# Performance work log

Measured on AMD Instinct MI355X. Metric: run time of the kernel, lower is better.

The kernel has to match this reference:

```python
import jax, jax.numpy as jnp
import numpy as np

B, S, D, H = 4, 2048, 768, 12
DH = D // H  # 64


def setup_inputs() -> dict:
    key = jax.random.key(0)
    ks = jax.random.split(key, 7)
    return {
        "sequences": jax.random.normal(ks[0], (B, S, D), dtype=jnp.float32),
        "wq": jax.random.normal(ks[1], (H, DH, DH), dtype=jnp.float32) / np.sqrt(DH),
        "bq": jax.random.normal(ks[2], (H, DH), dtype=jnp.float32) * 0.02,
        "wk": jax.random.normal(ks[3], (H, DH, DH), dtype=jnp.float32) / np.sqrt(DH),
        "bk": jax.random.normal(ks[4], (H, DH), dtype=jnp.float32) * 0.02,
        "wv": jax.random.normal(ks[5], (H, DH, DH), dtype=jnp.float32) / np.sqrt(DH),
        "bv": jax.random.normal(ks[6], (H, DH), dtype=jnp.float32) * 0.02,
    }


def reference(sequences, wq, bq, wk, bk, wv, bv):
    # split channels into heads: [B, S, H, DH]
    xh = sequences.reshape(B, S, H, DH)
    # per-head linear projections (weight applied as x @ W^T + b, matching nn.Linear)
    q = jnp.einsum("bshd,hed->bshe", xh, wq) + bq  # [B,S,H,DH]
    k = jnp.einsum("bshd,hed->bshe", xh, wk) + bk
    v = jnp.einsum("bshd,hed->bshe", xh, wv) + bv
    scale = 1.0 / np.sqrt(DH).astype(np.float32)
    scores = jnp.einsum("bqhd,bkhd->bhqk", q, k) * scale  # [B,H,S,S]
    attn = jax.nn.softmax(scores, axis=-1)
    out = jnp.einsum("bhqk,bkhd->bqhd", attn, v)  # [B,S,H,DH]
    return out.reshape(B, S, D)
```

## Files before the change

### kernel.cpp

```cpp
#include <hip/hip_runtime.h>

#define NB 4
#define NS 2048
#define ND 768
#define NH 12
#define NDH 64
#define XPITCH 72
#define SSCALE 0.18033688011112043f

typedef __bf16 bf16x8 __attribute__((ext_vector_type(8)));
typedef float  f32x4  __attribute__((ext_vector_type(4)));
typedef unsigned int u32;

#define MFMA16(a, b, c) __builtin_amdgcn_mfma_f32_16x16x32_bf16(a, b, c, 0, 0, 0)

__device__ __forceinline__ u32 packbf(float a, float b) {
    u32 ua = __builtin_bit_cast(u32, a) + 0x8000u;
    u32 ub = __builtin_bit_cast(u32, b) + 0x8000u;
    return __builtin_amdgcn_perm(ub, ua, 0x07060302u);
}

__device__ __forceinline__ bf16x8 cvt8(float4 a, float4 b) {
    union { u32 u[4]; bf16x8 v; } r;
    r.u[0] = packbf(a.x, a.y); r.u[1] = packbf(a.z, a.w);
    r.u[2] = packbf(b.x, b.y); r.u[3] = packbf(b.z, b.w);
    return r.v;
}

__device__ __forceinline__ __bf16 f2bf(float f) {
    u32 u = __builtin_bit_cast(u32, f) + 0x8000u;
    unsigned short s = (unsigned short)(u >> 16);
    return __builtin_bit_cast(__bf16, s);
}

__device__ __forceinline__ void gl16(const __bf16* g, __bf16* l) {
    __builtin_amdgcn_global_load_lds(
        (const __attribute__((address_space(1))) unsigned int*)g,
        (__attribute__((address_space(3))) unsigned int*)l,
        16, 0, 0);
}


__global__ __launch_bounds__(256, 3) void proj_kernel(
    const float* __restrict__ x,
    const float* __restrict__ wq, const float* __restrict__ bq,
    const float* __restrict__ wk, const float* __restrict__ bk,
    const float* __restrict__ wv, const float* __restrict__ bv,
    __bf16* __restrict__ qws, __bf16* __restrict__ kws, __bf16* __restrict__ vtws)
{
    const int stp = blockIdx.x, h = blockIdx.y, b = blockIdx.z;
    const int st0 = stp * 2, st1 = stp * 2 + 1;
    const int tid = threadIdx.x;

    __shared__ __align__(16) __bf16 Xs[2][64 * XPITCH];
    __shared__ __align__(16) __bf16 Tv[2][64 * XPITCH];

    const int r = tid >> 2, f = tid & 3;
    const int lane = tid & 63, w = tid >> 6, col = lane & 15, quad = lane >> 4;

    const size_t wrow = (size_t)(h * NDH + w * 16 + col) * NDH;
    const float* wq0 = wq + wrow + quad * 8;
    const float* wk0 = wk + wrow + quad * 8;
    const float* wv0 = wv + wrow + quad * 8;
    const bf16x8 wqa0 = cvt8(*(const float4*)(wq0),      *(const float4*)(wq0 + 4));
    const bf16x8 wqa1 = cvt8(*(const float4*)(wq0 + 32), *(const float4*)(wq0 + 36));
    const bf16x8 wka0 = cvt8(*(const float4*)(wk0),      *(const float4*)(wk0 + 4));
    const bf16x8 wka1 = cvt8(*(const float4*)(wk0 + 32), *(const float4*)(wk0 + 36));
    const bf16x8 wva0 = cvt8(*(const float4*)(wv0),      *(const float4*)(wv0 + 4));
    const bf16x8 wva1 = cvt8(*(const float4*)(wv0 + 32), *(const float4*)(wv0 + 36));

    float bqs[4], bks[4], bvs[4];
#pragma unroll
    for (int rr = 0; rr < 4; ++rr) {
        const int e = h * NDH + w * 16 + quad * 4 + rr;
        bqs[rr] = bq[e] * SSCALE;
        bks[rr] = bk[e];
        bvs[rr] = bv[e];
    }

    const size_t bh = (size_t)(b * NH + h);

    const int e0 = w * 16 + quad * 4;
    const int jj = e0 >> 5;
    const int qa = (e0 >> 3) & 3;
    const int hf = (e0 >> 2) & 1;
    const int Lf = qa * 16 + col;

    const float* xrow0 = x + (size_t)(b * NS + st0 * 64 + r) * ND + h * NDH + f * 16;
    const float* xrow1 = xrow0 + (size_t)64 * ND;
    {
        const float4 v0 = *(const float4*)(xrow0);
        const float4 v1 = *(const float4*)(xrow0 + 4);
        const float4 v2 = *(const float4*)(xrow0 + 8);
        const float4 v3 = *(const float4*)(xrow0 + 12);
        *(bf16x8*)&Xs[0][r * XPITCH + f * 16]     = cvt8(v0, v1);
        *(bf16x8*)&Xs[0][r * XPITCH + f * 16 + 8] = cvt8(v2, v3);
    }
    const float4 xn0 = *(const float4*)(xrow1);
    const float4 xn1 = *(const float4*)(xrow1 + 4);
    const float4 xn2 = *(const float4*)(xrow1 + 8);
    const float4 xn3 = *(const float4*)(xrow1 + 12);
    __syncthreads();

    auto do_tile = [&](int st, const __bf16* XsP, __bf16* TvP) {
        const int kt = st >> 1;
#pragma unroll
        for (int nt = 0; nt < 4; ++nt) {
            const bf16x8 xb0 = *(const bf16x8*)&XsP[(nt * 16 + col) * XPITCH + quad * 8];
            const bf16x8 xb1 = *(const bf16x8*)&XsP[(nt * 16 + col) * XPITCH + 32 + quad * 8];
            f32x4 aq = {0.f, 0.f, 0.f, 0.f};
            f32x4 ak = {0.f, 0.f, 0.f, 0.f};
            f32x4 av = {0.f, 0.f, 0.f, 0.f};
            aq = MFMA16(wqa0, xb0, aq); aq = MFMA16(wqa1, xb1, aq);
            ak = MFMA16(wka0, xb0, ak); ak = MFMA16(wka1, xb1, ak);
            av = MFMA16(wva0, xb0, av); av = MFMA16(wva1, xb1, av);

            union { u32 u[2]; uint2 v; } pq, pk;
            pq.u[0] = packbf(fmaf(aq[0], SSCALE, bqs[0]), fmaf(aq[1], SSCALE, bqs[1]));
            pq.u[1] = packbf(fmaf(aq[2], SSCALE, bqs[2]), fmaf(aq[3], SSCALE, bqs[3]));
            pk.u[0] = packbf(ak[0] + bks[0], ak[1] + bks[1]);
            pk.u[1] = packbf(ak[2] + bks[2], ak[3] + bks[3]);

            const int wa = (st & 1) * 2 + (nt >> 1);
            const int mt = nt & 1;
            const size_t kidx = ((((((size_t)bh * 16 + kt) * 4 + wa) * 2 + mt) * 2 + jj) * 64 + Lf) * 8 + hf * 4;
            const size_t qidx = (((((size_t)bh * 32 + st) * 4 + nt) * 2 + jj) * 64 + Lf) * 8 + hf * 4;
            *(uint2*)(kws + kidx) = pk.v;
            *(uint2*)(qws + qidx) = pq.v;

            const int pos = ((nt >> 1) << 5) + ((col >> 2) << 3) + ((nt & 1) << 2) + (col & 3);
#pragma unroll
            for (int rr = 0; rr < 4; ++rr)
                TvP[(w * 16 + quad * 4 + rr) * XPITCH + pos] = f2bf(av[rr] + bvs[rr]);
        }
    };

    auto v_store = [&](int st, const __bf16* TvP) {
        const uint4 v0 = *(const uint4*)&TvP[r * XPITCH + f * 16];
        const uint4 v1 = *(const uint4*)&TvP[r * XPITCH + f * 16 + 8];
        const int kt = st >> 1;
        const int wv_ = (st & 1) * 2 + (f >> 1);
        const int dtv = r >> 4;
        const int colv = r & 15;
        const int L0 = ((f & 1) * 2 + 0) * 16 + colv;
        const int L1 = ((f & 1) * 2 + 1) * 16 + colv;
        const size_t vbase = (((size_t)bh * 16 + kt) * 4 + wv_) * 4 + dtv;
        *(uint4*)(vtws + (vbase * 64 + L0) * 8) = v0;
        *(uint4*)(vtws + (vbase * 64 + L1) * 8) = v1;
    };

    do_tile(st0, Xs[0], Tv[0]);
    *(bf16x8*)&Xs[1][r * XPITCH + f * 16]     = cvt8(xn0, xn1);
    *(bf16x8*)&Xs[1][r * XPITCH + f * 16 + 8] = cvt8(xn2, xn3);
    __syncthreads();

    v_store(st0, Tv[0]);
    do_tile(st1, Xs[1], Tv[1]);
    __syncthreads();
    v_store(st1, Tv[1]);
}

__global__ __launch_bounds__(256, 4) void attn_kernel(
    const __bf16* __restrict__ qws, const __bf16* __restrict__ kws,
    const __bf16* __restrict__ vtws, float* __restrict__ out)
{
    const int bid = blockIdx.x;
    const int xcd = bid & 7;
    const int j   = bid >> 3;
    const int g   = xcd * 6 + (j >> 5);
    const int qt  = j & 31;
    const int h   = g % NH;
    const int b   = g / NH;

    const int q0 = qt * 64;
    const int tid = threadIdx.x;

    __shared__ __align__(16) unsigned char smem[32768];
    __bf16* ldsK = (__bf16*)smem;
    float* slab  = (float*)smem;
    float* lbuf  = (float*)(smem + 17408);

    const size_t bh = (size_t)(b * NH + h);
    const int lane = tid & 63, w = tid >> 6, col = lane & 15, quad = lane >> 4;
    const int wq = w >> 1, wk = w & 1;

    bf16x8 qb0[2], qb1[2];
    {
        const __bf16* qp = qws + (size_t)bh * 131072 + (size_t)qt * 4096
                         + wq * 2048 + lane * 8;
#pragma unroll
        for (int nt = 0; nt < 2; ++nt) {
            qb0[nt] = *(const bf16x8*)(qp + nt * 1024);
            qb1[nt] = *(const bf16x8*)(qp + nt * 1024 + 512);
        }
    }

    const __bf16* kg = kws  + (size_t)bh * 131072 + wk * 2048 + lane * 8;
    const __bf16* vg = vtws + (size_t)bh * 131072 + wk * 2048 + lane * 8;
    __bf16* lk0 = ldsK + w * 2048;
    __bf16* lk1 = ldsK + 8192 + w * 2048;
    const __bf16* lkr0 = lk0 + lane * 8;
    const __bf16* lkr1 = lk1 + lane * 8;

    float l[2] = {0.f, 0.f};
    f32x4 o[4][2];
#pragma unroll
    for (int dt = 0; dt < 4; ++dt)
#pragma unroll
        for (int nt = 0; nt < 2; ++nt) o[dt][nt] = (f32x4){0.f, 0.f, 0.f, 0.f};

#define ATTN_ITER(ktv, LKRD, LKN, DMA_C, PV_LAST) do {                        \
        const __bf16* _vp = vg + (size_t)(ktv) * 4096;                        \
        const bf16x8 va0 = *(const bf16x8*)(_vp);                             \
        const bf16x8 va1 = *(const bf16x8*)(_vp + 512);                       \
        const bf16x8 va2 = *(const bf16x8*)(_vp + 1024);                      \
        const bf16x8 va3 = *(const bf16x8*)(_vp + 1536);                      \
        if (DMA_C) {                                                          \
            const __bf16* _kn = kg + (size_t)((ktv) + 1) * 4096;              \
            gl16(_kn,        LKN);        gl16(_kn + 512,  LKN + 512);        \
            gl16(_kn + 1024, LKN + 1024); gl16(_kn + 1536, LKN + 1536);       \
        }                                                                     \
        __builtin_amdgcn_sched_barrier(0);                                    \
        if (DMA_C) { asm volatile("s_waitcnt vmcnt(8)" ::: "memory"); }       \
        else       { asm volatile("s_waitcnt vmcnt(4)" ::: "memory"); }       \
        __builtin_amdgcn_sched_barrier(0);                                    \
        const bf16x8 ka00 = *(const bf16x8*)(LKRD);                           \
        const bf16x8 ka01 = *(const bf16x8*)(LKRD + 512);                     \
        const bf16x8 ka10 = *(const bf16x8*)(LKRD + 1024);                    \
        const bf16x8 ka11 = *(const bf16x8*)(LKRD + 1536);                    \
        union { u32 u[4]; bf16x8 v; } pb[2];                                  \
        _Pragma("unroll")                                                     \
        for (int nt = 0; nt < 2; ++nt) {                                      \
            f32x4 sA = {0.f, 0.f, 0.f, 0.f};                                  \
            f32x4 sB = {0.f, 0.f, 0.f, 0.f};                                  \
            sA = MFMA16(ka00, qb0[nt], sA); sA = MFMA16(ka01, qb1[nt], sA);   \
            sB = MFMA16(ka10, qb0[nt], sB); sB = MFMA16(ka11, qb1[nt], sB);   \
            const float p0 = __builtin_amdgcn_exp2f(sA[0]);                   \
            const float p1 = __builtin_amdgcn_exp2f(sA[1]);                   \
            const float p2 = __builtin_amdgcn_exp2f(sA[2]);                   \
            const float p3 = __builtin_amdgcn_exp2f(sA[3]);                   \
            const float p4 = __builtin_amdgcn_exp2f(sB[0]);                   \
            const float p5 = __builtin_amdgcn_exp2f(sB[1]);                   \
            const float p6 = __builtin_amdgcn_exp2f(sB[2]);                   \
            const float p7 = __builtin_amdgcn_exp2f(sB[3]);                   \
            l[nt] += ((p0 + p1) + (p2 + p3)) + ((p4 + p5) + (p6 + p7));       \
            pb[nt].u[0] = packbf(p0, p1);                                     \
            pb[nt].u[1] = packbf(p2, p3);                                     \
            pb[nt].u[2] = packbf(p4, p5);                                     \
            pb[nt].u[3] = packbf(p6, p7);                                     \
        }                                                                     \
        __builtin_amdgcn_sched_barrier(0);                                    \
        if (PV_LAST) { asm volatile("s_waitcnt vmcnt(0)" ::: "memory"); }     \
        else         { asm volatile("s_waitcnt vmcnt(4)" ::: "memory"); }     \
        __builtin_amdgcn_sched_barrier(0);                                    \
        _Pragma("unroll")                                                     \
        for (int nt = 0; nt < 2; ++nt) {                                      \
            o[0][nt] = MFMA16(va0, pb[nt].v, o[0][nt]);                       \
            o[1][nt] = MFMA16(va1, pb[nt].v, o[1][nt]);                       \
            o[2][nt] = MFMA16(va2, pb[nt].v, o[2][nt]);                       \
            o[3][nt] = MFMA16(va3, pb[nt].v, o[3][nt]);                       \
        }                                                                     \
    } while (0)

    gl16(kg,        lk0);        gl16(kg + 512,  lk0 + 512);
    gl16(kg + 1024, lk0 + 1024); gl16(kg + 1536, lk0 + 1536);

    for (int kt2 = 0; kt2 < 30; kt2 += 2) {
        ATTN_ITER(kt2,     lkr0, lk1, true, false);
        ATTN_ITER(kt2 + 1, lkr1, lk0, true, false);
    }
    ATTN_ITER(30, lkr0, lk1, true,  false);
    ATTN_ITER(31, lkr1, lk0, false, true);
#undef ATTN_ITER

#pragma unroll
    for (int nt = 0; nt < 2; ++nt) {
        l[nt] += __shfl_xor(l[nt], 16, 64);
        l[nt] += __shfl_xor(l[nt], 32, 64);
    }

    __syncthreads();
    if (quad == 0) {
#pragma unroll
        for (int nt = 0; nt < 2; ++nt)
            lbuf[wk * 64 + wq * 32 + nt * 16 + col] = l[nt];
    }
    __syncthreads();

    float scale[2];
#pragma unroll
    for (int nt = 0; nt < 2; ++nt) {
        const int ri = wq * 32 + nt * 16 + col;
        scale[nt] = 1.0f / (lbuf[ri] + lbuf[64 + ri]);
    }
#pragma unroll
    for (int dt = 0; dt < 4; ++dt)
#pragma unroll
        for (int nt = 0; nt < 2; ++nt) o[dt][nt] *= scale[nt];

    if (wk == 0) {
#pragma unroll
        for (int dt = 0; dt < 4; ++dt)
#pragma unroll
            for (int nt = 0; nt < 2; ++nt)
                *(f32x4*)&slab[(wq * 32 + nt * 16 + col) * 68 + dt * 16 + quad * 4] = o[dt][nt];
    }
    __syncthreads();
    if (wk == 1) {
#pragma unroll
        for (int dt = 0; dt < 4; ++dt)
#pragma unroll
            for (int nt = 0; nt < 2; ++nt) {
                f32x4* p = (f32x4*)&slab[(wq * 32 + nt * 16 + col) * 68 + dt * 16 + quad * 4];
                *p = *p + o[dt][nt];
            }
    }
    __syncthreads();

    const int qr = tid >> 2, fq = tid & 3;
#pragma unroll
    for (int j2 = 0; j2 < 4; ++j2) {
        const f32x4 a = *(const f32x4*)&slab[qr * 68 + fq * 16 + j2 * 4];
        *(f32x4*)&out[(size_t)(b * NS + q0 + qr) * ND + h * NDH + fq * 16 + j2 * 4] = a;
    }
}

extern "C" void kernel_launch(void* const* d_in, const int* in_sizes, int n_in,
                              void* d_out, int out_size, void* d_ws, size_t ws_size,
                              hipStream_t stream) {
    (void)in_sizes; (void)n_in; (void)out_size; (void)ws_size;
    const float* x  = (const float*)d_in[0];
    const float* wq = (const float*)d_in[1];
    const float* bq = (const float*)d_in[2];
    const float* wk = (const float*)d_in[3];
    const float* bk = (const float*)d_in[4];
    const float* wv = (const float*)d_in[5];
    const float* bv = (const float*)d_in[6];
    float* out = (float*)d_out;

    __bf16* qws  = (__bf16*)d_ws;
    __bf16* kws  = qws + (size_t)NB * NH * NS * NDH;
    __bf16* vtws = kws + (size_t)NB * NH * NS * NDH;

    proj_kernel<<<dim3(NS / 128, NH, NB), 256, 0, stream>>>(x, wq, bq, wk, bk, wv, bv, qws, kws, vtws);
    attn_kernel<<<dim3(NS / 64 * NH * NB), 256, 0, stream>>>(qws, kws, vtws, out);
}
```

Measured before the change: 160.6 us.

## Give each wave its own query rows and drop split-K cross-wave reduction

```diff
diff --git a/kernel.cpp b/kernel.cpp
--- a/kernel.cpp
+++ b/kernel.cpp
@@ -167,27 +167,23 @@
     const int bid = blockIdx.x;
     const int xcd = bid & 7;
     const int j   = bid >> 3;
-    const int g   = xcd * 6 + (j >> 5);
-    const int qt  = j & 31;
+    const int g   = xcd * 6 + (j >> 4);
+    const int qtp = j & 15;
     const int h   = g % NH;
     const int b   = g / NH;
 
-    const int q0 = qt * 64;
     const int tid = threadIdx.x;
 
     __shared__ __align__(16) unsigned char smem[32768];
     __bf16* ldsK = (__bf16*)smem;
-    float* slab  = (float*)smem;
-    float* lbuf  = (float*)(smem + 17408);
 
     const size_t bh = (size_t)(b * NH + h);
     const int lane = tid & 63, w = tid >> 6, col = lane & 15, quad = lane >> 4;
-    const int wq = w >> 1, wk = w & 1;
 
     bf16x8 qb0[2], qb1[2];
     {
-        const __bf16* qp = qws + (size_t)bh * 131072 + (size_t)qt * 4096
-                         + wq * 2048 + lane * 8;
+        const __bf16* qp = qws + (size_t)bh * 131072 + (size_t)(qtp * 2 + (w >> 1)) * 4096
+                         + (w & 1) * 2048 + lane * 8;
 #pragma unroll
         for (int nt = 0; nt < 2; ++nt) {
             qb0[nt] = *(const bf16x8*)(qp + nt * 1024);
@@ -195,8 +191,8 @@
         }
     }
 
-    const __bf16* kg = kws  + (size_t)bh * 131072 + wk * 2048 + lane * 8;
-    const __bf16* vg = vtws + (size_t)bh * 131072 + wk * 2048 + lane * 8;
+    const __bf16* kg = kws  + (size_t)bh * 131072 + lane * 8;
+    const __bf16* vg = vtws + (size_t)bh * 131072 + lane * 8;
     __bf16* lk0 = ldsK + w * 2048;
     __bf16* lk1 = ldsK + 8192 + w * 2048;
     const __bf16* lkr0 = lk0 + lane * 8;
@@ -210,13 +206,13 @@
         for (int nt = 0; nt < 2; ++nt) o[dt][nt] = (f32x4){0.f, 0.f, 0.f, 0.f};
 
 #define ATTN_ITER(ktv, LKRD, LKN, DMA_C, PV_LAST) do {                        \
-        const __bf16* _vp = vg + (size_t)(ktv) * 4096;                        \
+        const __bf16* _vp = vg + (size_t)(ktv) * 2048;                        \
         const bf16x8 va0 = *(const bf16x8*)(_vp);                             \
         const bf16x8 va1 = *(const bf16x8*)(_vp + 512);                       \
         const bf16x8 va2 = *(const bf16x8*)(_vp + 1024);                      \
         const bf16x8 va3 = *(const bf16x8*)(_vp + 1536);                      \
         if (DMA_C) {                                                          \
-            const __bf16* _kn = kg + (size_t)((ktv) + 1) * 4096;              \
+            const __bf16* _kn = kg + (size_t)((ktv) + 1) * 2048;              \
             gl16(_kn,        LKN);        gl16(_kn + 512,  LKN + 512);        \
             gl16(_kn + 1024, LKN + 1024); gl16(_kn + 1536, LKN + 1536);       \
         }                                                                     \
@@ -265,12 +261,12 @@
     gl16(kg,        lk0);        gl16(kg + 512,  lk0 + 512);
     gl16(kg + 1024, lk0 + 1024); gl16(kg + 1536, lk0 + 1536);
 
-    for (int kt2 = 0; kt2 < 30; kt2 += 2) {
+    for (int kt2 = 0; kt2 < 62; kt2 += 2) {
         ATTN_ITER(kt2,     lkr0, lk1, true, false);
         ATTN_ITER(kt2 + 1, lkr1, lk0, true, false);
     }
-    ATTN_ITER(30, lkr0, lk1, true,  false);
-    ATTN_ITER(31, lkr1, lk0, false, true);
+    ATTN_ITER(62, lkr0, lk1, true,  false);
+    ATTN_ITER(63, lkr1, lk0, false, true);
 #undef ATTN_ITER
 
 #pragma unroll
@@ -279,50 +275,19 @@
         l[nt] += __shfl_xor(l[nt], 32, 64);
     }
 
-    __syncthreads();
-    if (quad == 0) {
-#pragma unroll
-        for (int nt = 0; nt < 2; ++nt)
-            lbuf[wk * 64 + wq * 32 + nt * 16 + col] = l[nt];
-    }
-    __syncthreads();
-
     float scale[2];
 #pragma unroll
-    for (int nt = 0; nt < 2; ++nt) {
-        const int ri = wq * 32 + nt * 16 + col;
-        scale[nt] = 1.0f / (lbuf[ri] + lbuf[64 + ri]);
-    }
+    for (int nt = 0; nt < 2; ++nt) scale[nt] = 1.0f / l[nt];
+
+    const int qrow0 = qtp * 128 + w * 32;
 #pragma unroll
     for (int dt = 0; dt < 4; ++dt)
 #pragma unroll
-        for (int nt = 0; nt < 2; ++nt) o[dt][nt] *= scale[nt];
-
-    if (wk == 0) {
-#pragma unroll
-        for (int dt = 0; dt < 4; ++dt)
-#pragma unroll
-            for (int nt = 0; nt < 2; ++nt)
-                *(f32x4*)&slab[(wq * 32 + nt * 16 + col) * 68 + dt * 16 + quad * 4] = o[dt][nt];
-    }
-    __syncthreads();
-    if (wk == 1) {
-#pragma unroll
-        for (int dt = 0; dt < 4; ++dt)
-#pragma unroll
-            for (int nt = 0; nt < 2; ++nt) {
-                f32x4* p = (f32x4*)&slab[(wq * 32 + nt * 16 + col) * 68 + dt * 16 + quad * 4];
-                *p = *p + o[dt][nt];
-            }
-    }
-    __syncthreads();
-
-    const int qr = tid >> 2, fq = tid & 3;
-#pragma unroll
-    for (int j2 = 0; j2 < 4; ++j2) {
-        const f32x4 a = *(const f32x4*)&slab[qr * 68 + fq * 16 + j2 * 4];
-        *(f32x4*)&out[(size_t)(b * NS + q0 + qr) * ND + h * NDH + fq * 16 + j2 * 4] = a;
-    }
+        for (int nt = 0; nt < 2; ++nt) {
+            const f32x4 r = o[dt][nt] * scale[nt];
+            *(f32x4*)&out[(size_t)(b * NS + qrow0 + nt * 16 + col) * ND
+                          + h * NDH + dt * 16 + quad * 4] = r;
+        }
 }
 
 extern "C" void kernel_launch(void* const* d_in, const int* in_sizes, int n_in,
@@ -343,5 +308,5 @@
     __bf16* vtws = kws + (size_t)NB * NH * NS * NDH;
 
     proj_kernel<<<dim3(NS / 128, NH, NB), 256, 0, stream>>>(x, wq, bq, wk, bk, wv, bv, qws, kws, vtws);
-    attn_kernel<<<dim3(NS / 64 * NH * NB), 256, 0, stream>>>(qws, kws, vtws, out);
-}
+    attn_kernel<<<dim3(768), 256, 0, stream>>>(qws, kws, vtws, out);
+}
```

Result: no change. 161.7 us (+0.7%).
